# Optimization experiments

Measured on AMD Instinct MI355X. Metric: run time of the kernel, lower is better.

Reference implementation:

```python
import jax, jax.numpy as jnp
import numpy as np

N_SIDE = 64            # regular RBF kernel grid: 64^3 kernels
LC0_DIM = 32
CMIN, CMAX = -1.0, 1.0
COMBS = [(0, 1), (0, 2), (1, 2)]
# 2^3 cell-corner offsets for the 8 nearest regular-grid kernels
OFFS = np.array([[i, j, k] for i in (0, 1) for j in (0, 1) for k in (0, 1)], dtype=np.int32)


def grid_sample_2d(plane, coords):
    """Bilinear, align_corners=True. plane [C,H,W]; coords [N,2] in [-1,1];
    coords[:,0] indexes W, coords[:,1] indexes H (torch grid_sample convention)."""
    C, H, W = plane.shape
    x = (coords[:, 0] + 1.0) * 0.5 * (W - 1)
    y = (coords[:, 1] + 1.0) * 0.5 * (H - 1)
    x0 = jnp.clip(jnp.floor(x), 0, W - 2).astype(jnp.int32)
    y0 = jnp.clip(jnp.floor(y), 0, H - 2).astype(jnp.int32)
    wx = (x - x0)[None, :]
    wy = (y - y0)[None, :]
    p00 = plane[:, y0, x0]
    p01 = plane[:, y0, x0 + 1]
    p10 = plane[:, y0 + 1, x0]
    p11 = plane[:, y0 + 1, x0 + 1]
    out = p00 * (1 - wx) * (1 - wy) + p01 * wx * (1 - wy) + p10 * (1 - wx) * wy + p11 * wx * wy
    return out.T  # [N,C]


def rbf_features(x, lc0, ks):
    """Regular-grid kNN (8 cell corners) + inverse-quadratic RBF weighting of local codes."""
    interval = (CMAX - CMIN) / (N_SIDE - 1)
    cell = jnp.clip(jnp.floor((x - CMIN) / interval), 0, N_SIDE - 2).astype(jnp.int32)  # [N,3]
    corner = cell[:, None, :] + jnp.asarray(OFFS)[None]                                  # [N,8,3]
    idx = (corner[..., 0] * N_SIDE + corner[..., 1]) * N_SIDE + corner[..., 2]           # [N,8]
    kc = CMIN + corner.astype(x.dtype) * interval                                        # [N,8,3] kernel centers
    d2 = jnp.sum((x[:, None, :] - kc) ** 2, axis=-1)                                     # [N,8]
    s = ks[idx]                                                                          # [N,8] per-kernel shape
    phi = 1.0 / (1.0 + d2 * s * s)                                                       # ivq RBF
    phi = phi / (jnp.sum(phi, axis=-1, keepdims=True) + 1e-8)                            # rbf_lc0_normalize
    codes = lc0[idx]                                                                     # [N,8,LC0_DIM]
    return jnp.einsum('nk,nkd->nd', phi, codes)


def setup_inputs() -> dict:
    key = jax.random.key(0)
    ks_ = jax.random.split(key, 16)
    N = 524288
    aabb = jnp.array([[-1.5, -1.5, -1.5], [1.5, 1.5, 1.5]], dtype=jnp.float32)
    pts = jax.random.uniform(ks_[0], (N, 3), minval=-1.5, maxval=1.5, dtype=jnp.float32)

    def plane(k, r):  # kp_init uniform(0.1, 0.5)
        return jax.random.uniform(k, (32, r, r), minval=0.1, maxval=0.5, dtype=jnp.float32)

    resos = [128, 256, 512]
    inp = {'pts': pts, 'aabb': aabb}
    ki = 1
    for si, r in enumerate(resos):
        for ci in range(3):
            inp[f'p{si}{ci}'] = plane(ks_[ki], r)
            ki += 1
    inp['lc0'] = jax.random.uniform(ks_[ki], (N_SIDE ** 3, LC0_DIM), minval=-1e-4, maxval=1e-4, dtype=jnp.float32)
    interval = (CMAX - CMIN) / (N_SIDE - 1)
    inp['ks'] = jnp.full((N_SIDE ** 3,), 1.0 / interval, dtype=jnp.float32)  # ks_alpha=1.0
    inp['kpb'] = jax.random.uniform(ks_[ki + 1], (96 + LC0_DIM,), minval=-1e-4, maxval=1e-4, dtype=jnp.float32)
    return inp


def reference(pts, aabb, p00, p01, p02, p10, p11, p12, p20, p21, p22, lc0, ks, kpb):
    planes = [[p00, p01, p02], [p10, p11, p12], [p20, p21, p22]]
    # normalize_aabb -> [-1,1]
    x = (pts - aabb[0]) * (2.0 / (aabb[1] - aabb[0])) - 1.0
    # interpolate_ms_features: product over planes within a scale, concat across scales
    feats = []
    for scale in planes:
        interp = 1.0
        for pl, comb in zip(scale, COMBS):
            interp = interp * grid_sample_2d(pl, x[:, list(comb)])
        feats.append(interp)
    kp = jnp.concatenate(feats, axis=-1)          # [N,96]
    rbf = rbf_features(x, lc0, ks)                # [N,32]
    return jnp.concatenate([kp, rbf], axis=-1) + kpb  # [N,128], + kpb bias
```

## Files before the change

kernel.cpp:

```cpp
#include <hip/hip_runtime.h>
#include <hip/hip_bf16.h>
#include <stdint.h>

typedef __hip_bfloat16 bf16;
typedef __hip_bfloat162 bf162;

#define S0 ((size_t)(128*128*32))
#define S1 ((size_t)(256*256*32))
#define S2 ((size_t)(512*512*32))
#define LCN ((size_t)(64*64*64*32))

#define T128 (128*128/64)
#define T256 (256*256/64)
#define T512 (512*512/64)
#define TPLANES (3*T128 + 3*T256 + 3*T512)
#define TLC ((int)(LCN/1024))

__global__ __launch_bounds__(256) void prepass_kernel(
    const float* __restrict__ p00, const float* __restrict__ p01, const float* __restrict__ p02,
    const float* __restrict__ p10, const float* __restrict__ p11, const float* __restrict__ p12,
    const float* __restrict__ p20, const float* __restrict__ p21, const float* __restrict__ p22,
    const float* __restrict__ lc0,
    bf16* __restrict__ tp0, bf16* __restrict__ tp1, bf16* __restrict__ tp2,
    bf16* __restrict__ lc0b)
{
    const int b = blockIdx.x;
    const int tid = threadIdx.x;
    if (b < TPLANES) {
        const float* src; bf16* dst; int HW, tile;
        if (b < 3 * T128) {
            int pid = b >> 8; tile = b & (T128 - 1); HW = 128 * 128;
            src = pid == 0 ? p00 : (pid == 1 ? p01 : p02);
            dst = tp0 + (size_t)pid * S0;
        } else if (b < 3 * T128 + 3 * T256) {
            int bb = b - 3 * T128; int pid = bb >> 10; tile = bb & (T256 - 1); HW = 256 * 256;
            src = pid == 0 ? p10 : (pid == 1 ? p11 : p12);
            dst = tp1 + (size_t)pid * S1;
        } else {
            int bb = b - 3 * T128 - 3 * T256; int pid = bb >> 12; tile = bb & (T512 - 1); HW = 512 * 512;
            src = pid == 0 ? p20 : (pid == 1 ? p21 : p22);
            dst = tp2 + (size_t)pid * S2;
        }
        const int base = tile * 64;
        __shared__ float t[64 * 33];
#pragma unroll
        for (int i = 0; i < 8; ++i) {
            int idx = i * 256 + tid;
            int c = idx >> 6, p = idx & 63;
            t[p * 33 + c] = src[(size_t)c * HW + base + p];
        }
        __syncthreads();
#pragma unroll
        for (int i = 0; i < 8; ++i) {
            int idx = i * 256 + tid;
            int p = idx >> 5, c = idx & 31;
            dst[(size_t)base * 32 + idx] = __float2bfloat16(t[p * 33 + c]);
        }
    } else {
        size_t off = (size_t)(b - TPLANES) * 1024 + (size_t)tid * 4;
        float4 v = *(const float4*)(lc0 + off);
        bf162* d = (bf162*)(lc0b + off);
        d[0] = __halves2bfloat162(__float2bfloat16(v.x), __float2bfloat16(v.y));
        d[1] = __halves2bfloat162(__float2bfloat16(v.z), __float2bfloat16(v.w));
    }
}

template <int R>
__device__ __forceinline__ float2 sample_tp(const bf162* __restrict__ tp,
                                            float cx, float cy, int cpair)
{
    float gx = (cx + 1.0f) * (0.5f * (float)(R - 1));
    float gy = (cy + 1.0f) * (0.5f * (float)(R - 1));
    float fx = fminf(fmaxf(floorf(gx), 0.0f), (float)(R - 2));
    float fy = fminf(fmaxf(floorf(gy), 0.0f), (float)(R - 2));
    float wx = gx - fx, wy = gy - fy;
    int ix = (int)fx, iy = (int)fy;
    size_t i00 = ((size_t)(iy * R + ix)) * 16 + cpair;
    bf162 v00 = tp[i00];
    bf162 v01 = tp[i00 + 16];
    bf162 v10 = tp[i00 + (size_t)R * 16];
    bf162 v11 = tp[i00 + (size_t)R * 16 + 16];
    float w11 = wx * wy;
    float w01 = wx - w11;
    float w10 = wy - w11;
    float w00 = 1.0f - wx - wy + w11;
    float2 r;
    r.x = __bfloat162float(v00.x) * w00 + __bfloat162float(v01.x) * w01
        + __bfloat162float(v10.x) * w10 + __bfloat162float(v11.x) * w11;
    r.y = __bfloat162float(v00.y) * w00 + __bfloat162float(v01.y) * w01
        + __bfloat162float(v10.y) * w10 + __bfloat162float(v11.y) * w11;
    return r;
}

template <int R>
__device__ __forceinline__ float2 plane_feat(const bf162* __restrict__ tp,
                                             float xn, float yn, float zn, int cpair)
{
    const size_t ps = (size_t)R * R * 16;
    float2 a = sample_tp<R>(tp,          xn, yn, cpair);
    float2 b = sample_tp<R>(tp + ps,     xn, zn, cpair);
    float2 c = sample_tp<R>(tp + 2 * ps, yn, zn, cpair);
    float2 r; r.x = a.x * b.x * c.x; r.y = a.y * b.y * c.y;
    return r;
}

__device__ __forceinline__ float2 sample_f32(const float* __restrict__ pl, int R,
                                             float cx, float cy, int ch)
{
    float gx = (cx + 1.0f) * 0.5f * (float)(R - 1);
    float gy = (cy + 1.0f) * 0.5f * (float)(R - 1);
    float fx = fminf(fmaxf(floorf(gx), 0.0f), (float)(R - 2));
    float fy = fminf(fmaxf(floorf(gy), 0.0f), (float)(R - 2));
    float wx = gx - fx, wy = gy - fy;
    int ix = (int)fx, iy = (int)fy;
    float w11 = wx * wy, w01 = wx - w11, w10 = wy - w11, w00 = 1.0f - wx - wy + w11;
    size_t HW = (size_t)R * R;
    const float* q0 = pl + (size_t)ch * HW + (size_t)iy * R + ix;
    const float* q1 = q0 + HW;
    float2 r;
    r.x = q0[0] * w00 + q0[1] * w01 + q0[R] * w10 + q0[R + 1] * w11;
    r.y = q1[0] * w00 + q1[1] * w01 + q1[R] * w10 + q1[R + 1] * w11;
    return r;
}

template <bool TP>
__device__ __forceinline__ float2 rbf_feat(const bf162* __restrict__ lc0b,
                                           const float* __restrict__ lc0f,
                                           const float* __restrict__ ks,
                                           float xn, float yn, float zn, int cpair)
{
    const float interval = 2.0f / 63.0f;
    const float invi = 31.5f;
    float fc0 = fminf(fmaxf(floorf((xn + 1.0f) * invi), 0.0f), 62.0f);
    float fc1 = fminf(fmaxf(floorf((yn + 1.0f) * invi), 0.0f), 62.0f);
    float fc2 = fminf(fmaxf(floorf((zn + 1.0f) * invi), 0.0f), 62.0f);
    int c0 = (int)fc0, c1 = (int)fc1, c2 = (int)fc2;
    float dx0 = xn - (-1.0f + fc0 * interval), dx1 = dx0 - interval;
    float dy0 = yn - (-1.0f + fc1 * interval), dy1 = dy0 - interval;
    float dz0 = zn - (-1.0f + fc2 * interval), dz1 = dz0 - interval;
    int ibase = (c0 * 64 + c1) * 64 + c2;

    float phi[8]; int id[8];
    float sum = 0.0f;
#pragma unroll
    for (int k = 0; k < 8; ++k) {
        int i = (k >> 2) & 1, j = (k >> 1) & 1, l = k & 1;
        int idx = ibase + i * 4096 + j * 64 + l;
        id[k] = idx;
        float ddx = i ? dx1 : dx0;
        float ddy = j ? dy1 : dy0;
        float ddz = l ? dz1 : dz0;
        float dd = ddx * ddx + ddy * ddy + ddz * ddz;
        float s = ks[idx];
        float ph = __builtin_amdgcn_rcpf(fmaf(dd, s * s, 1.0f));
        phi[k] = ph;
        sum += ph;
    }
    float inv = __builtin_amdgcn_rcpf(sum + 1e-8f);
    float ax = 0.0f, ay = 0.0f;
#pragma unroll
    for (int k = 0; k < 8; ++k) {
        float w = phi[k] * inv;
        float vx, vy;
        if (TP) {
            bf162 v = lc0b[(size_t)id[k] * 16 + cpair];
            vx = __bfloat162float(v.x); vy = __bfloat162float(v.y);
        } else {
            const float* cp = lc0f + (size_t)id[k] * 32 + 2 * cpair;
            vx = cp[0]; vy = cp[1];
        }
        ax = fmaf(w, vx, ax);
        ay = fmaf(w, vy, ay);
    }
    float2 r; r.x = ax; r.y = ay;
    return r;
}

template <bool TP>
__global__ __launch_bounds__(256) void field_kernel(
    const float* __restrict__ pts, const float* __restrict__ aabb,
    const float* __restrict__ p00, const float* __restrict__ p01, const float* __restrict__ p02,
    const float* __restrict__ p10, const float* __restrict__ p11, const float* __restrict__ p12,
    const float* __restrict__ p20, const float* __restrict__ p21, const float* __restrict__ p22,
    const bf162* __restrict__ tp0, const bf162* __restrict__ tp1, const bf162* __restrict__ tp2,
    const bf162* __restrict__ lc0b, const float* __restrict__ lc0f,
    const float* __restrict__ ks, const float* __restrict__ kpb,
    float* __restrict__ out, int N)
{
    const int wave  = threadIdx.x >> 6;
    const int lane  = threadIdx.x & 63;
    const int p     = lane >> 4;
    const int cpair = lane & 15;
    const int n = blockIdx.x * 4 + p;
    if (n >= N) return;

    float px = pts[3 * (size_t)n + 0];
    float py = pts[3 * (size_t)n + 1];
    float pz = pts[3 * (size_t)n + 2];
    float xn = (px - aabb[0]) * (2.0f / (aabb[3] - aabb[0])) - 1.0f;
    float yn = (py - aabb[1]) * (2.0f / (aabb[4] - aabb[1])) - 1.0f;
    float zn = (pz - aabb[2]) * (2.0f / (aabb[5] - aabb[2])) - 1.0f;

    float2 val;
    int f;
    if (wave == 0) {
        if (TP) val = plane_feat<128>(tp0, xn, yn, zn, cpair);
        else {
            float2 a = sample_f32(p00, 128, xn, yn, 2 * cpair);
            float2 b = sample_f32(p01, 128, xn, zn, 2 * cpair);
            float2 c = sample_f32(p02, 128, yn, zn, 2 * cpair);
            val.x = a.x * b.x * c.x; val.y = a.y * b.y * c.y;
        }
        f = 2 * cpair;
    } else if (wave == 1) {
        if (TP) val = plane_feat<256>(tp1, xn, yn, zn, cpair);
        else {
            float2 a = sample_f32(p10, 256, xn, yn, 2 * cpair);
            float2 b = sample_f32(p11, 256, xn, zn, 2 * cpair);
            float2 c = sample_f32(p12, 256, yn, zn, 2 * cpair);
            val.x = a.x * b.x * c.x; val.y = a.y * b.y * c.y;
        }
        f = 32 + 2 * cpair;
    } else if (wave == 2) {
        if (TP) val = plane_feat<512>(tp2, xn, yn, zn, cpair);
        else {
            float2 a = sample_f32(p20, 512, xn, yn, 2 * cpair);
            float2 b = sample_f32(p21, 512, xn, zn, 2 * cpair);
            float2 c = sample_f32(p22, 512, yn, zn, 2 * cpair);
            val.x = a.x * b.x * c.x; val.y = a.y * b.y * c.y;
        }
        f = 64 + 2 * cpair;
    } else {
        val = rbf_feat<TP>(lc0b, lc0f, ks, xn, yn, zn, cpair);
        f = 96 + 2 * cpair;
    }

    val.x += kpb[f];
    val.y += kpb[f + 1];
    *(float2*)(out + (size_t)n * 128 + f) = val;
}

extern "C" void kernel_launch(void* const* d_in, const int* in_sizes, int n_in,
                              void* d_out, int out_size, void* d_ws, size_t ws_size,
                              hipStream_t stream)
{
    const float* pts  = (const float*)d_in[0];
    const float* aabb = (const float*)d_in[1];
    const float* pl[9];
    for (int i = 0; i < 9; ++i) pl[i] = (const float*)d_in[2 + i];
    const float* lc0 = (const float*)d_in[11];
    const float* ks  = (const float*)d_in[12];
    const float* kpb = (const float*)d_in[13];
    float* out = (float*)d_out;
    const int N = in_sizes[0] / 3;

    const size_t need = (3 * (S0 + S1 + S2) + LCN) * sizeof(bf16);
    bf16* w    = (bf16*)d_ws;
    bf16* tp0  = w;
    bf16* tp1  = tp0 + 3 * S0;
    bf16* tp2  = tp1 + 3 * S1;
    bf16* lc0b = tp2 + 3 * S2;

    const bool useTP = (d_ws != nullptr) && (ws_size >= need);
    const int blocks = (N + 3) / 4;

    if (useTP) {
        prepass_kernel<<<TPLANES + TLC, 256, 0, stream>>>(
            pl[0], pl[1], pl[2], pl[3], pl[4], pl[5], pl[6], pl[7], pl[8],
            lc0, tp0, tp1, tp2, lc0b);
        field_kernel<true><<<blocks, 256, 0, stream>>>(
            pts, aabb, pl[0], pl[1], pl[2], pl[3], pl[4], pl[5], pl[6], pl[7], pl[8],
            (const bf162*)tp0, (const bf162*)tp1, (const bf162*)tp2,
            (const bf162*)lc0b, lc0, ks, kpb, out, N);
    } else {
        field_kernel<false><<<blocks, 256, 0, stream>>>(
            pts, aabb, pl[0], pl[1], pl[2], pl[3], pl[4], pl[5], pl[6], pl[7], pl[8],
            (const bf162*)d_ws, (const bf162*)d_ws, (const bf162*)d_ws,
            (const bf162*)d_ws, lc0, ks, kpb, out, N);
    }
}
```

Baseline: 700.2 us.

## Bucket-sort points by Morton cell before field sampling for gather locality

Adds a counting sort of points into 32^3 Morton-ordered buckets: a count pass fused into the prepass, a single-block scan, and an atomic scatter writing normalized coords plus the original index. The field kernel then reads sorted points and remaps block IDs across 8 groups, so nearby points share plane and lc0 cache lines. It also writes output at scattered rows. This costs extra launches, atomics, a serial scan and N*16 bytes of workspace. Output rows become non-contiguous per block, and the block remap may spread concurrently running blocks across different regions.

```diff
diff --git a/kernel.cpp b/kernel.cpp
--- a/kernel.cpp
+++ b/kernel.cpp
@@ -15,6 +15,30 @@
 #define T512 (512*512/64)
 #define TPLANES (3*T128 + 3*T256 + 3*T512)
 #define TLC ((int)(LCN/1024))
+
+#define NBUCKETS 32768
+
+__device__ __forceinline__ uint32_t mpart(uint32_t x)
+{
+    x = (x | (x << 16)) & 0x030000FFu;
+    x = (x | (x << 8))  & 0x0300F00Fu;
+    x = (x | (x << 4))  & 0x030C30C3u;
+    x = (x | (x << 2))  & 0x09249249u;
+    return x;
+}
+
+__device__ __forceinline__ uint32_t bucket_of(float xn, float yn, float zn)
+{
+    float bx = fminf(fmaxf(floorf((xn + 1.0f) * 16.0f), 0.0f), 31.0f);
+    float by = fminf(fmaxf(floorf((yn + 1.0f) * 16.0f), 0.0f), 31.0f);
+    float bz = fminf(fmaxf(floorf((zn + 1.0f) * 16.0f), 0.0f), 31.0f);
+    return mpart((uint32_t)bx) | (mpart((uint32_t)by) << 1) | (mpart((uint32_t)bz) << 2);
+}
+
+__global__ __launch_bounds__(256) void zero_counts_kernel(unsigned int* __restrict__ counts)
+{
+    counts[blockIdx.x * 256 + threadIdx.x] = 0u;
+}
 
 __global__ __launch_bounds__(256) void prepass_kernel(
     const float* __restrict__ p00, const float* __restrict__ p01, const float* __restrict__ p02,
@@ -22,10 +46,13 @@
     const float* __restrict__ p20, const float* __restrict__ p21, const float* __restrict__ p22,
     const float* __restrict__ lc0,
     bf16* __restrict__ tp0, bf16* __restrict__ tp1, bf16* __restrict__ tp2,
-    bf16* __restrict__ lc0b)
+    bf16* __restrict__ lc0b,
+    const float* __restrict__ pts, const float* __restrict__ aabb,
+    unsigned int* __restrict__ counts, int N)
 {
     const int b = blockIdx.x;
     const int tid = threadIdx.x;
+    __shared__ float t[64 * 33];
     if (b < TPLANES) {
         const float* src; bf16* dst; int HW, tile;
         if (b < 3 * T128) {
@@ -42,7 +69,6 @@
             dst = tp2 + (size_t)pid * S2;
         }
         const int base = tile * 64;
-        __shared__ float t[64 * 33];
 #pragma unroll
         for (int i = 0; i < 8; ++i) {
             int idx = i * 256 + tid;
@@ -56,13 +82,62 @@
             int p = idx >> 5, c = idx & 31;
             dst[(size_t)base * 32 + idx] = __float2bfloat16(t[p * 33 + c]);
         }
-    } else {
+    } else if (b < TPLANES + TLC) {
         size_t off = (size_t)(b - TPLANES) * 1024 + (size_t)tid * 4;
         float4 v = *(const float4*)(lc0 + off);
         bf162* d = (bf162*)(lc0b + off);
         d[0] = __halves2bfloat162(__float2bfloat16(v.x), __float2bfloat16(v.y));
         d[1] = __halves2bfloat162(__float2bfloat16(v.z), __float2bfloat16(v.w));
-    }
+    } else {
+        int idx = (b - TPLANES - TLC) * 256 + tid;
+        if (idx < N) {
+            float px = pts[3 * (size_t)idx + 0];
+            float py = pts[3 * (size_t)idx + 1];
+            float pz = pts[3 * (size_t)idx + 2];
+            float xn = (px - aabb[0]) * (2.0f / (aabb[3] - aabb[0])) - 1.0f;
+            float yn = (py - aabb[1]) * (2.0f / (aabb[4] - aabb[1])) - 1.0f;
+            float zn = (pz - aabb[2]) * (2.0f / (aabb[5] - aabb[2])) - 1.0f;
+            atomicAdd(&counts[bucket_of(xn, yn, zn)], 1u);
+        }
+    }
+}
+
+__global__ __launch_bounds__(1024) void scan_kernel(unsigned int* __restrict__ counts)
+{
+    __shared__ unsigned int sums[1024];
+    const int t = threadIdx.x;
+    unsigned int local[32];
+    unsigned int s = 0;
+#pragma unroll
+    for (int i = 0; i < 32; ++i) { local[i] = counts[t * 32 + i]; s += local[i]; }
+    sums[t] = s;
+    __syncthreads();
+    for (int off = 1; off < 1024; off <<= 1) {
+        unsigned int v = (t >= off) ? sums[t - off] : 0u;
+        __syncthreads();
+        sums[t] += v;
+        __syncthreads();
+    }
+    unsigned int run = sums[t] - s;
+#pragma unroll
+    for (int i = 0; i < 32; ++i) { unsigned int c = local[i]; counts[t * 32 + i] = run; run += c; }
+}
+
+__global__ __launch_bounds__(256) void scatter_kernel(
+    const float* __restrict__ pts, const float* __restrict__ aabb,
+    unsigned int* __restrict__ offsets, float4* __restrict__ sp, int N)
+{
+    int n = blockIdx.x * 256 + threadIdx.x;
+    if (n >= N) return;
+    float px = pts[3 * (size_t)n + 0];
+    float py = pts[3 * (size_t)n + 1];
+    float pz = pts[3 * (size_t)n + 2];
+    float xn = (px - aabb[0]) * (2.0f / (aabb[3] - aabb[0])) - 1.0f;
+    float yn = (py - aabb[1]) * (2.0f / (aabb[4] - aabb[1])) - 1.0f;
+    float zn = (pz - aabb[2]) * (2.0f / (aabb[5] - aabb[2])) - 1.0f;
+    unsigned int pos = atomicAdd(&offsets[bucket_of(xn, yn, zn)], 1u);
+    float4 v; v.x = xn; v.y = yn; v.z = zn; v.w = __int_as_float(n);
+    sp[pos] = v;
 }
 
 template <int R>
@@ -176,7 +251,7 @@
     return r;
 }
 
-template <bool TP>
+template <bool TP, bool SORTED>
 __global__ __launch_bounds__(256) void field_kernel(
     const float* __restrict__ pts, const float* __restrict__ aabb,
     const float* __restrict__ p00, const float* __restrict__ p01, const float* __restrict__ p02,
@@ -185,21 +260,35 @@
     const bf162* __restrict__ tp0, const bf162* __restrict__ tp1, const bf162* __restrict__ tp2,
     const bf162* __restrict__ lc0b, const float* __restrict__ lc0f,
     const float* __restrict__ ks, const float* __restrict__ kpb,
+    const float4* __restrict__ sp,
     float* __restrict__ out, int N)
 {
     const int wave  = threadIdx.x >> 6;
     const int lane  = threadIdx.x & 63;
     const int p     = lane >> 4;
     const int cpair = lane & 15;
-    const int n = blockIdx.x * 4 + p;
-    if (n >= N) return;
-
-    float px = pts[3 * (size_t)n + 0];
-    float py = pts[3 * (size_t)n + 1];
-    float pz = pts[3 * (size_t)n + 2];
-    float xn = (px - aabb[0]) * (2.0f / (aabb[3] - aabb[0])) - 1.0f;
-    float yn = (py - aabb[1]) * (2.0f / (aabb[4] - aabb[1])) - 1.0f;
-    float zn = (pz - aabb[2]) * (2.0f / (aabb[5] - aabb[2])) - 1.0f;
+    int bid = blockIdx.x;
+    if (SORTED) {
+        int nb = gridDim.x;
+        if ((nb & 7) == 0) bid = (bid & 7) * (nb >> 3) + (bid >> 3);
+    }
+    const int m = bid * 4 + p;
+    if (m >= N) return;
+
+    float xn, yn, zn;
+    int n;
+    if (SORTED) {
+        float4 q = sp[m];
+        xn = q.x; yn = q.y; zn = q.z; n = __float_as_int(q.w);
+    } else {
+        n = m;
+        float px = pts[3 * (size_t)n + 0];
+        float py = pts[3 * (size_t)n + 1];
+        float pz = pts[3 * (size_t)n + 2];
+        xn = (px - aabb[0]) * (2.0f / (aabb[3] - aabb[0])) - 1.0f;
+        yn = (py - aabb[1]) * (2.0f / (aabb[4] - aabb[1])) - 1.0f;
+        zn = (pz - aabb[2]) * (2.0f / (aabb[5] - aabb[2])) - 1.0f;
+    }
 
     float2 val;
     int f;
@@ -254,28 +343,47 @@
     float* out = (float*)d_out;
     const int N = in_sizes[0] / 3;
 
-    const size_t need = (3 * (S0 + S1 + S2) + LCN) * sizeof(bf16);
+    const size_t needTP = (3 * (S0 + S1 + S2) + LCN) * sizeof(bf16);
+    const size_t cntOff = needTP;
+    const size_t spOff  = cntOff + (size_t)NBUCKETS * 4;
+    const size_t needSort = spOff + (size_t)N * 16;
+
     bf16* w    = (bf16*)d_ws;
     bf16* tp0  = w;
     bf16* tp1  = tp0 + 3 * S0;
     bf16* tp2  = tp1 + 3 * S1;
     bf16* lc0b = tp2 + 3 * S2;
-
-    const bool useTP = (d_ws != nullptr) && (ws_size >= need);
+    unsigned int* counts = (unsigned int*)((char*)d_ws + cntOff);
+    float4* sp = (float4*)((char*)d_ws + spOff);
+
+    const bool useTP   = (d_ws != nullptr) && (ws_size >= needTP);
+    const bool useSort = (d_ws != nullptr) && (ws_size >= needSort);
     const int blocks = (N + 3) / 4;
-
-    if (useTP) {
+    const int cntBlocks = (N + 255) / 256;
+
+    if (useSort) {
+        zero_counts_kernel<<<NBUCKETS / 256, 256, 0, stream>>>(counts);
+        prepass_kernel<<<TPLANES + TLC + cntBlocks, 256, 0, stream>>>(
+            pl[0], pl[1], pl[2], pl[3], pl[4], pl[5], pl[6], pl[7], pl[8],
+            lc0, tp0, tp1, tp2, lc0b, pts, aabb, counts, N);
+        scan_kernel<<<1, 1024, 0, stream>>>(counts);
+        scatter_kernel<<<cntBlocks, 256, 0, stream>>>(pts, aabb, counts, sp, N);
+        field_kernel<true, true><<<blocks, 256, 0, stream>>>(
+            pts, aabb, pl[0], pl[1], pl[2], pl[3], pl[4], pl[5], pl[6], pl[7], pl[8],
+            (const bf162*)tp0, (const bf162*)tp1, (const bf162*)tp2,
+            (const bf162*)lc0b, lc0, ks, kpb, sp, out, N);
+    } else if (useTP) {
         prepass_kernel<<<TPLANES + TLC, 256, 0, stream>>>(
             pl[0], pl[1], pl[2], pl[3], pl[4], pl[5], pl[6], pl[7], pl[8],
-            lc0, tp0, tp1, tp2, lc0b);
-        field_kernel<true><<<blocks, 256, 0, stream>>>(
+            lc0, tp0, tp1, tp2, lc0b, pts, aabb, nullptr, 0);
+        field_kernel<true, false><<<blocks, 256, 0, stream>>>(
             pts, aabb, pl[0], pl[1], pl[2], pl[3], pl[4], pl[5], pl[6], pl[7], pl[8],
             (const bf162*)tp0, (const bf162*)tp1, (const bf162*)tp2,
-            (const bf162*)lc0b, lc0, ks, kpb, out, N);
+            (const bf162*)lc0b, lc0, ks, kpb, nullptr, out, N);
     } else {
-        field_kernel<false><<<blocks, 256, 0, stream>>>(
+        field_kernel<false, false><<<blocks, 256, 0, stream>>>(
             pts, aabb, pl[0], pl[1], pl[2], pl[3], pl[4], pl[5], pl[6], pl[7], pl[8],
             (const bf162*)d_ws, (const bf162*)d_ws, (const bf162*)d_ws,
-            (const bf162*)d_ws, lc0, ks, kpb, out, N);
-    }
-}
+            (const bf162*)d_ws, lc0, ks, kpb, nullptr, out, N);
+    }
+}
```

New measurement: 601.8 us. 14.0% less time.
